# Kernel tuning notes

Hardware: AMD Instinct MI355X
Metric: run time of the kernel (lower is better)

The kernel has to match this reference:

```python
import jax, jax.numpy as jnp
import numpy as np

N = 100000      # num_nodes
E = 1600000     # num_edges (avg degree 16)
D_IN = 128
D_H = 128
D_OUT = 128


def _init_linear(key, out_dim, in_dim):
    # Kaiming-uniform-like init, bound = 1/sqrt(fan_in)
    bound = 1.0 / np.sqrt(in_dim)
    return jax.random.uniform(key, (out_dim, in_dim), jnp.float32, -bound, bound)


def setup_inputs() -> dict:
    key = jax.random.key(0)
    ks = jax.random.split(key, 12)
    x = jax.random.normal(ks[0], (N, D_IN), jnp.float32)
    edge_index = jax.random.randint(ks[1], (2, E), 0, N, jnp.int32)
    dims = [(D_H, D_IN), (D_H, D_H), (D_OUT, D_H)]
    inp = {"x": x, "edge_index": edge_index}
    for i, (do, di) in enumerate(dims):
        inp[f"Wl{i}"] = _init_linear(ks[2 + 3 * i], do, di)      # lin_l: applied to aggregated neighbors
        inp[f"bl{i}"] = jnp.zeros((do,), jnp.float32)
        inp[f"Wr{i}"] = _init_linear(ks[3 + 3 * i], do, di)      # lin_r: applied to root (self) features
    return inp


def _sage_conv(x, src, dst, Wl, bl, Wr):
    # mean aggregation of source-node features at destination nodes
    msg = x[src]                                                   # [E, d]
    agg = jax.ops.segment_sum(msg, dst, num_segments=N)            # [N, d]
    deg = jax.ops.segment_sum(jnp.ones((src.shape[0],), x.dtype), dst, num_segments=N)
    mean = agg / jnp.maximum(deg, 1.0)[:, None]
    return mean @ Wl.T + bl + x @ Wr.T


def reference(x, edge_index, Wl0, bl0, Wr0, Wl1, bl1, Wr1, Wl2, bl2, Wr2):
    src, dst = edge_index[0], edge_index[1]
    # dropout is identity in eval mode
    h = jax.nn.relu(_sage_conv(x, src, dst, Wl0, bl0, Wr0))
    h = jax.nn.relu(_sage_conv(h, src, dst, Wl1, bl1, Wr1))
    return _sage_conv(h, src, dst, Wl2, bl2, Wr2)
```

## Files before the change

### kernel.cpp

```cpp
#include <hip/hip_runtime.h>
#include <hip/hip_bf16.h>

typedef __attribute__((ext_vector_type(8))) short bf16x8;
typedef __attribute__((ext_vector_type(4))) float f32x4;
typedef __attribute__((ext_vector_type(2))) float f32x2;

#define D 128
#define BCAP 8192
#define EPB 3125
#define SBMAX 512


__global__ __launch_bounds__(256) void k_mega(
    const float* __restrict__ x,
    const float* __restrict__ w0, const float* __restrict__ w1,
    const float* __restrict__ w2, const float* __restrict__ w3,
    const float* __restrict__ w4, const float* __restrict__ w5,
    __hip_bfloat16* __restrict__ xb, __hip_bfloat16* __restrict__ wb,
    __hip_bfloat16* __restrict__ h0,
    int* __restrict__ gbuf, int* __restrict__ runinfo,
    const int* __restrict__ src, const int* __restrict__ dst,
    int xquad, int e, int n, int p1b)
{
    if (blockIdx.x < p1b) {
        __shared__ int lh[512], lpre[512], pscan[256];
        __shared__ int lout[3328];
        int t = threadIdx.x;
        lh[t] = 0; lh[t + 256] = 0;
        __syncthreads();
        int lo = blockIdx.x * EPB;
        int hi = lo + EPB; if (hi > e) hi = e;
        for (int i = lo + t; i < hi; i += 256) {
            int d = dst[i]; d = ((unsigned)d < (unsigned)n) ? d : 0;
            atomicAdd(&lh[d >> 8], 1);
        }
        __syncthreads();
        int c0 = lh[2 * t], c1 = lh[2 * t + 1];
        int pair = c0 + c1;
        pscan[t] = pair;
        __syncthreads();
        for (int off = 1; off < 256; off <<= 1) {
            int v = (t >= off) ? pscan[t - off] : 0;
            __syncthreads();
            pscan[t] += v;
            __syncthreads();
        }
        int excl = pscan[t] - pair;
        lpre[2 * t] = excl;
        lpre[2 * t + 1] = excl + c0;
        runinfo[(2 * t) * SBMAX + blockIdx.x]     = (excl << 16) | c0;
        runinfo[(2 * t + 1) * SBMAX + blockIdx.x] = ((excl + c0) << 16) | c1;
        lh[2 * t] = 0; lh[2 * t + 1] = 0;
        __syncthreads();
        for (int i = lo + t; i < hi; i += 256) {
            int d = dst[i]; d = ((unsigned)d < (unsigned)n) ? d : 0;
            int s = src[i]; s = ((unsigned)s < (unsigned)n) ? s : 0;
            int b = d >> 8;
            int p = lpre[b] + atomicAdd(&lh[b], 1);
            lout[p] = s | ((d & 255) << 17);
        }
        __syncthreads();
        int cnt = hi - lo;
        for (int i = t; i < cnt; i += 256) gbuf[lo + i] = lout[i];
    } else {
        int t = (blockIdx.x - p1b) * 256 + threadIdx.x;
        if (t < xquad) {
            float4 f = ((const float4*)x)[t];
            union { int2 i2; __hip_bfloat162 h2[2]; } u;
            u.h2[0] = __float22bfloat162_rn(make_float2(f.x, f.y));
            u.h2[1] = __float22bfloat162_rn(make_float2(f.z, f.w));
            ((int2*)xb)[t] = u.i2;
        }
        if (t < 6 * 4096) {
            int wsel = t >> 12, wi = t & 4095;
            const float* wp = w0;
            if (wsel == 1) wp = w1;
            else if (wsel == 2) wp = w2;
            else if (wsel == 3) wp = w3;
            else if (wsel == 4) wp = w4;
            else if (wsel == 5) wp = w5;
            float4 f = ((const float4*)wp)[wi];
            union { int2 i2; __hip_bfloat162 h2[2]; } u;
            u.h2[0] = __float22bfloat162_rn(make_float2(f.x, f.y));
            u.h2[1] = __float22bfloat162_rn(make_float2(f.z, f.w));
            ((int2*)wb)[t] = u.i2;
        }
        if (t < 16) {
            ((int4*)(xb + (size_t)n * D))[t] = make_int4(0, 0, 0, 0);
            ((int4*)(h0 + (size_t)n * D))[t] = make_int4(0, 0, 0, 0);
        }
    }
}


__global__ __launch_bounds__(256) void k_p2(
    const int* __restrict__ gbuf, const int* __restrict__ runinfo,
    int2* __restrict__ ndesc,
    int* __restrict__ csr, int n, int p1b)
{
    __shared__ int ebuf[BCAP];
    __shared__ int out[BCAP];
    __shared__ int pscan[256];
    __shared__ int hist[256], loc[256], cur[256];
    int b = blockIdx.x, t = threadIdx.x;

    int sb0 = 2 * t, sb1 = 2 * t + 1;
    int r0 = (sb0 < p1b) ? runinfo[b * SBMAX + sb0] : 0;
    int r1 = (sb1 < p1b) ? runinfo[b * SBMAX + sb1] : 0;
    int l0 = r0 & 0xffff, l1 = r1 & 0xffff;
    int pair = l0 + l1;
    pscan[t] = pair;
    __syncthreads();
    for (int off = 1; off < 256; off <<= 1) {
        int v = (t >= off) ? pscan[t - off] : 0;
        __syncthreads();
        pscan[t] += v;
        __syncthreads();
    }
    int excl = pscan[t] - pair;
    int cnt = pscan[255];
    if (cnt > BCAP) cnt = BCAP;

    if (excl < BCAP) {
        int s0 = sb0 * EPB + (r0 >> 16);
        int lim0 = (excl + l0 <= BCAP) ? l0 : (BCAP - excl);
        for (int k = 0; k < lim0; ++k) ebuf[excl + k] = gbuf[s0 + k];
        int o1 = excl + l0;
        if (o1 < BCAP) {
            int s1 = sb1 * EPB + (r1 >> 16);
            int lim1 = (o1 + l1 <= BCAP) ? l1 : (BCAP - o1);
            for (int k = 0; k < lim1; ++k) ebuf[o1 + k] = gbuf[s1 + k];
        }
    }
    __syncthreads();

    int nodes = n - b * 256; if (nodes > 256) nodes = 256;
    hist[t] = 0;
    __syncthreads();
    for (int i = t; i < cnt; i += 256)
        atomicAdd(&hist[(ebuf[i] >> 17) & 255], 1);
    __syncthreads();
    int v = hist[t];
    int pv = (v + 15) & ~15;
    loc[t] = pv;
    __syncthreads();
    for (int off = 1; off < 256; off <<= 1) {
        int x = (t >= off) ? loc[t - off] : 0;
        __syncthreads();
        loc[t] += x;
        __syncthreads();
    }
    int myloc = loc[t] - pv;
    int ptot = loc[255];
    if (ptot > BCAP) ptot = BCAP;
    cur[t] = myloc;
    if (t < nodes) ndesc[b * 256 + t] = make_int2(b * BCAP + myloc, v);
    __syncthreads();
    for (int i = t; i < ptot; i += 256) out[i] = n;
    __syncthreads();
    for (int i = t; i < cnt; i += 256) {
        int ed = ebuf[i];
        int p = atomicAdd(&cur[(ed >> 17) & 255], 1);
        if (p < BCAP) out[p] = ed & 0x1FFFF;
    }
    __syncthreads();
    for (int i = t; i < ptot; i += 256) csr[b * BCAP + i] = out[i];
}


__device__ __forceinline__ void acc_u32(f32x2& a, unsigned p) {
    f32x2 c;
    c.x = __uint_as_float(p << 16);
    c.y = __uint_as_float(p & 0xffff0000u);
    a += c;
}

__device__ __forceinline__ void acc_i4(f32x2* acc, int4 d) {
    acc_u32(acc[0], (unsigned)d.x);
    acc_u32(acc[1], (unsigned)d.y);
    acc_u32(acc[2], (unsigned)d.z);
    acc_u32(acc[3], (unsigned)d.w);
}

__global__ __launch_bounds__(256) void k_agg(
    const __hip_bfloat16* __restrict__ h,
    const int* __restrict__ csr,
    const int2* __restrict__ ndesc,
    __hip_bfloat16* __restrict__ mean,
    int n)
{
    int node = blockIdx.x * 4 + (threadIdx.x >> 6);
    int lane = threadIdx.x & 63;
    if (node >= n) return;
    int grp = lane >> 4;
    int sub = lane & 15;
    int2 nd = ndesc[node];
    int start = nd.x, cnt = nd.y;
    int cntp = (cnt + 15) & ~15;

    f32x2 acc[4];
    #pragma unroll
    for (int k = 0; k < 4; ++k) acc[k] = (f32x2){0.f, 0.f};

    const char* hb = (const char*)h;
    unsigned suboff = (unsigned)sub * 16u;
    const int* cp = csr + start + grp;

    for (int i = 0; i < cntp; i += 16) {
        int s[4];
        #pragma unroll
        for (int u = 0; u < 4; ++u) s[u] = cp[i + u * 4];
        int4 d[4];
        #pragma unroll
        for (int u = 0; u < 4; ++u)
            d[u] = *(const int4*)(hb + (((unsigned)s[u] << 8) | suboff));
        #pragma unroll
        for (int u = 0; u < 4; ++u) acc_i4(acc, d[u]);
    }

    #pragma unroll
    for (int k = 0; k < 4; ++k) {
        acc[k].x += __shfl_xor(acc[k].x, 16);
        acc[k].y += __shfl_xor(acc[k].y, 16);
        acc[k].x += __shfl_xor(acc[k].x, 32);
        acc[k].y += __shfl_xor(acc[k].y, 32);
    }

    if (grp == 0) {
        float inv = 1.0f / fmaxf((float)cnt, 1.0f);
        union { int4 i4; __hip_bfloat162 h2[4]; } u;
        #pragma unroll
        for (int k = 0; k < 4; ++k)
            u.h2[k] = __float22bfloat162_rn(make_float2(acc[k].x * inv, acc[k].y * inv));
        *(int4*)((char*)mean + (size_t)node * 256 + suboff) = u.i4;
    }
}


__global__ __launch_bounds__(512) void k_gemm(
    const __hip_bfloat16* __restrict__ A0,
    const __hip_bfloat16* __restrict__ A1,
    const __hip_bfloat16* __restrict__ Wb,
    const float* __restrict__ bias,
    float* __restrict__ outF,
    __hip_bfloat16* __restrict__ outB,
    int n, int do_relu)
{
    __shared__ __hip_bfloat16 lW[2 * 128 * 128];

    for (int g = threadIdx.x; g < 4096; g += 512) {
        int half = g >> 11;
        int rem  = g & 2047;
        int row  = rem >> 4;
        int c    = rem & 15;
        bf16x8 v = *(const bf16x8*)(Wb + half * 16384 + row * 128 + c * 8);
        *(bf16x8*)(lW + half * 16384 + row * 128 + ((c ^ (row & 7)) * 8)) = v;
    }
    __syncthreads();

    int w = threadIdx.x >> 6;
    int lane = threadIdx.x & 63;
    int m = lane & 15;
    int q = lane >> 4;
    int base = blockIdx.x * 256 + w * 32;

    f32x4 acc[2][8];
    #pragma unroll
    for (int r = 0; r < 2; ++r)
        #pragma unroll
        for (int i = 0; i < 8; ++i) acc[r][i] = (f32x4){0.f, 0.f, 0.f, 0.f};

    const __hip_bfloat16* Aps[2] = {A0, A1};

    #pragma unroll
    for (int half = 0; half < 2; ++half) {
        const __hip_bfloat16* A = Aps[half];
        #pragma unroll
        for (int kk = 0; kk < 4; ++kk) {
            bf16x8 af[2];
            #pragma unroll
            for (int r = 0; r < 2; ++r) {
                int arow = base + r * 16 + m;
                if (arow > n - 1) arow = n - 1;
                af[r] = *(const bf16x8*)(A + (size_t)arow * D + kk * 32 + q * 8);
            }
            #pragma unroll
            for (int nt = 0; nt < 8; ++nt) {
                int row = nt * 16 + m;
                int c = (kk * 4 + q) ^ (m & 7);
                bf16x8 bf = *(const bf16x8*)(lW + half * 16384 + row * 128 + c * 8);
                #pragma unroll
                for (int r = 0; r < 2; ++r)
                    acc[r][nt] = __builtin_amdgcn_mfma_f32_16x16x32_bf16(af[r], bf, acc[r][nt], 0, 0, 0);
            }
        }
    }

    #pragma unroll
    for (int r = 0; r < 2; ++r) {
        #pragma unroll
        for (int nt = 0; nt < 8; ++nt) {
            int col = nt * 16 + m;
            float b = bias[col];
            #pragma unroll
            for (int rr = 0; rr < 4; ++rr) {
                int row = base + r * 16 + q * 4 + rr;
                if (row < n) {
                    float v = acc[r][nt][rr] + b;
                    if (do_relu) v = fmaxf(v, 0.f);
                    if (outF) outF[(size_t)row * D + col] = v;
                    else      outB[(size_t)row * D + col] = __float2bfloat16(v);
                }
            }
        }
    }
}


extern "C" void kernel_launch(void* const* d_in, const int* in_sizes, int n_in,
                              void* d_out, int out_size, void* d_ws, size_t ws_size,
                              hipStream_t stream) {
    const float* x   = (const float*)d_in[0];
    const int*   ei  = (const int*)d_in[1];
    const float* Wl0 = (const float*)d_in[2];
    const float* bl0 = (const float*)d_in[3];
    const float* Wr0 = (const float*)d_in[4];
    const float* Wl1 = (const float*)d_in[5];
    const float* bl1 = (const float*)d_in[6];
    const float* Wr1 = (const float*)d_in[7];
    const float* Wl2 = (const float*)d_in[8];
    const float* bl2 = (const float*)d_in[9];
    const float* Wr2 = (const float*)d_in[10];

    const int n = in_sizes[0] / D;
    const int e = in_sizes[1] / 2;
    const int* src = ei;
    const int* dst = ei + e;
    const int nb = (n + 255) >> 8;

    uintptr_t p = ((uintptr_t)d_ws + 255) & ~(uintptr_t)255;
    auto carve = [&](size_t bytes) {
        uintptr_t r = p;
        p = (p + bytes + 255) & ~(uintptr_t)255;
        return (void*)r;
    };
    int2* ndesc  = (int2*)carve((size_t)n * 8);
    __hip_bfloat16* mean = (__hip_bfloat16*)carve((size_t)n * D * 2);
    __hip_bfloat16* F1   = (__hip_bfloat16*)carve((size_t)(n + 1) * D * 2);
    __hip_bfloat16* Wb   = (__hip_bfloat16*)carve((size_t)6 * D * D * 2);
    (void)ws_size; (void)n_in; (void)out_size;

    char* ob = (char*)d_out;
    __hip_bfloat16* h0 = (__hip_bfloat16*)ob;
    size_t hbytes = (size_t)(n + 1) * D * 2;
    int* gbuf    = (int*)(ob + hbytes);
    int* runinfo = (int*)(ob + hbytes + (size_t)e * 4);
    int* csrS    = (int*)(ob + hbytes + (size_t)e * 4 + (size_t)SBMAX * 512 * 4);

    const int xquad = n * D / 4;
    const int p1b = (e + EPB - 1) / EPB;

    const int megag = p1b + (xquad + 255) / 256;
    k_mega<<<megag, 256, 0, stream>>>(
        x, Wl0, Wr0, Wl1, Wr1, Wl2, Wr2, F1, Wb, h0, gbuf, runinfo, src, dst,
        xquad, e, n, p1b);

    k_p2<<<nb, 256, 0, stream>>>(gbuf, runinfo, ndesc, csrS, n, p1b);

    const int ag = (n + 3) / 4;
    const int gg = (n + 255) / 256;

    __hip_bfloat16* Wb0 = Wb + 0 * 2 * D * D;
    __hip_bfloat16* Wb1 = Wb + 1 * 2 * D * D;
    __hip_bfloat16* Wb2 = Wb + 2 * 2 * D * D;

    k_agg<<<ag, 256, 0, stream>>>(F1, csrS, ndesc, mean, n);
    k_gemm<<<gg, 512, 0, stream>>>(mean, F1, Wb0, bl0, nullptr, h0, n, 1);
    k_agg<<<ag, 256, 0, stream>>>(h0, csrS, ndesc, mean, n);
    k_gemm<<<gg, 512, 0, stream>>>(mean, h0, Wb1, bl1, nullptr, F1, n, 1);
    k_agg<<<ag, 256, 0, stream>>>(F1, csrS, ndesc, mean, n);
    k_gemm<<<gg, 512, 0, stream>>>(mean, F1, Wb2, bl2, (float*)d_out, nullptr, n, 0);
}
```

Baseline: 370.7 us.

## Pre-swizzle weights into MFMA fragment order and drop LDS staging in GEMM

The weight conversion in the mega kernel now writes bf16 weights directly in the per-lane MFMA B-fragment order. The GEMM kernel then loads B fragments straight from global memory (served mostly from L2/L1), so it no longer fills a 64KB LDS tile and syncs. The GEMM block is halved to 256 threads covering 128 rows, with an occupancy hint. This removes the per-block LDS fill and barrier overhead and the LDS occupancy limit, but adds repeated global or cache loads of the weights per wave.

```diff
diff --git a/kernel.cpp b/kernel.cpp
--- a/kernel.cpp
+++ b/kernel.cpp
@@ -71,19 +71,28 @@
             u.h2[1] = __float22bfloat162_rn(make_float2(f.z, f.w));
             ((int2*)xb)[t] = u.i2;
         }
-        if (t < 6 * 4096) {
-            int wsel = t >> 12, wi = t & 4095;
+        if (t < 6 * 2048) {
+            int mat   = t >> 11;
+            int piece = t & 2047;
+            int kk = piece >> 9;
+            int nt = (piece >> 6) & 7;
+            int l  = piece & 63;
+            int row = nt * 16 + (l & 15);
+            int col = kk * 32 + (l >> 4) * 8;
             const float* wp = w0;
-            if (wsel == 1) wp = w1;
-            else if (wsel == 2) wp = w2;
-            else if (wsel == 3) wp = w3;
-            else if (wsel == 4) wp = w4;
-            else if (wsel == 5) wp = w5;
-            float4 f = ((const float4*)wp)[wi];
-            union { int2 i2; __hip_bfloat162 h2[2]; } u;
-            u.h2[0] = __float22bfloat162_rn(make_float2(f.x, f.y));
-            u.h2[1] = __float22bfloat162_rn(make_float2(f.z, f.w));
-            ((int2*)wb)[t] = u.i2;
+            if (mat == 1) wp = w1;
+            else if (mat == 2) wp = w2;
+            else if (mat == 3) wp = w3;
+            else if (mat == 4) wp = w4;
+            else if (mat == 5) wp = w5;
+            const float4* s4 = (const float4*)(wp + row * 128 + col);
+            float4 f0 = s4[0], f1 = s4[1];
+            union { bf16x8 v; __hip_bfloat162 h2[4]; } u;
+            u.h2[0] = __float22bfloat162_rn(make_float2(f0.x, f0.y));
+            u.h2[1] = __float22bfloat162_rn(make_float2(f0.z, f0.w));
+            u.h2[2] = __float22bfloat162_rn(make_float2(f1.x, f1.y));
+            u.h2[3] = __float22bfloat162_rn(make_float2(f1.z, f1.w));
+            *(bf16x8*)(wb + mat * 16384 + piece * 8) = u.v;
         }
         if (t < 16) {
             ((int4*)(xb + (size_t)n * D))[t] = make_int4(0, 0, 0, 0);
@@ -237,32 +246,20 @@
 }
 
 
-__global__ __launch_bounds__(512) void k_gemm(
+__global__ __launch_bounds__(256, 4) void k_gemm(
     const __hip_bfloat16* __restrict__ A0,
     const __hip_bfloat16* __restrict__ A1,
-    const __hip_bfloat16* __restrict__ Wb,
+    const __hip_bfloat16* __restrict__ WbF,
     const float* __restrict__ bias,
     float* __restrict__ outF,
     __hip_bfloat16* __restrict__ outB,
     int n, int do_relu)
 {
-    __shared__ __hip_bfloat16 lW[2 * 128 * 128];
-
-    for (int g = threadIdx.x; g < 4096; g += 512) {
-        int half = g >> 11;
-        int rem  = g & 2047;
-        int row  = rem >> 4;
-        int c    = rem & 15;
-        bf16x8 v = *(const bf16x8*)(Wb + half * 16384 + row * 128 + c * 8);
-        *(bf16x8*)(lW + half * 16384 + row * 128 + ((c ^ (row & 7)) * 8)) = v;
-    }
-    __syncthreads();
-
     int w = threadIdx.x >> 6;
     int lane = threadIdx.x & 63;
     int m = lane & 15;
     int q = lane >> 4;
-    int base = blockIdx.x * 256 + w * 32;
+    int base = blockIdx.x * 128 + w * 32;
 
     f32x4 acc[2][8];
     #pragma unroll
@@ -275,6 +272,7 @@
     #pragma unroll
     for (int half = 0; half < 2; ++half) {
         const __hip_bfloat16* A = Aps[half];
+        const __hip_bfloat16* Wf = WbF + half * 16384 + lane * 8;
         #pragma unroll
         for (int kk = 0; kk < 4; ++kk) {
             bf16x8 af[2];
@@ -286,9 +284,7 @@
             }
             #pragma unroll
             for (int nt = 0; nt < 8; ++nt) {
-                int row = nt * 16 + m;
-                int c = (kk * 4 + q) ^ (m & 7);
-                bf16x8 bf = *(const bf16x8*)(lW + half * 16384 + row * 128 + c * 8);
+                bf16x8 bf = *(const bf16x8*)(Wf + (kk * 512 + nt * 64) * 8);
                 #pragma unroll
                 for (int r = 0; r < 2; ++r)
                     acc[r][nt] = __builtin_amdgcn_mfma_f32_16x16x32_bf16(af[r], bf, acc[r][nt], 0, 0, 0);
@@ -368,16 +364,16 @@
     k_p2<<<nb, 256, 0, stream>>>(gbuf, runinfo, ndesc, csrS, n, p1b);
 
     const int ag = (n + 3) / 4;
-    const int gg = (n + 255) / 256;
+    const int gg = (n + 127) / 128;
 
     __hip_bfloat16* Wb0 = Wb + 0 * 2 * D * D;
     __hip_bfloat16* Wb1 = Wb + 1 * 2 * D * D;
     __hip_bfloat16* Wb2 = Wb + 2 * 2 * D * D;
 
     k_agg<<<ag, 256, 0, stream>>>(F1, csrS, ndesc, mean, n);
-    k_gemm<<<gg, 512, 0, stream>>>(mean, F1, Wb0, bl0, nullptr, h0, n, 1);
+    k_gemm<<<gg, 256, 0, stream>>>(mean, F1, Wb0, bl0, nullptr, h0, n, 1);
     k_agg<<<ag, 256, 0, stream>>>(h0, csrS, ndesc, mean, n);
-    k_gemm<<<gg, 512, 0, stream>>>(mean, h0, Wb1, bl1, nullptr, F1, n, 1);
+    k_gemm<<<gg, 256, 0, stream>>>(mean, h0, Wb1, bl1, nullptr, F1, n, 1);
     k_agg<<<ag, 256, 0, stream>>>(F1, csrS, ndesc, mean, n);
-    k_gemm<<<gg, 512, 0, stream>>>(mean, F1, Wb2, bl2, (float*)d_out, nullptr, n, 0);
-}
+    k_gemm<<<gg, 256, 0, stream>>>(mean, F1, Wb2, bl2, (float*)d_out, nullptr, n, 0);
+}
```

After: 389.5 us. 5.1% more time.

## Shrink GEMM tiles to 64 rows with staged half-weight LDS and move buffers to workspace

Applied to the files above, without the earlier changes.

The fused GEMM now uses 256-thread blocks covering 64 rows, with each wave computing one 16-row tile. It stages only half of the weight matrix (32 KB) in LDS at a time and reloads it between the neighbor half and the self half. The aim is to raise occupancy and the number of blocks in flight (about 1563 instead of 391), at the cost of loading weights more often per output row and an extra barrier. Scratch buffers (h0, gbuf, runinfo, csrS) move from the output buffer into the workspace, which also removes the aliasing of h0 with the final output.

```diff
diff --git a/kernel.cpp b/kernel.cpp
--- a/kernel.cpp
+++ b/kernel.cpp
@@ -237,7 +237,7 @@
 }
 
 
-__global__ __launch_bounds__(512) void k_gemm(
+__global__ __launch_bounds__(256) void k_gemm(
     const __hip_bfloat16* __restrict__ A0,
     const __hip_bfloat16* __restrict__ A1,
     const __hip_bfloat16* __restrict__ Wb,
@@ -246,71 +246,59 @@
     __hip_bfloat16* __restrict__ outB,
     int n, int do_relu)
 {
-    __shared__ __hip_bfloat16 lW[2 * 128 * 128];
-
-    for (int g = threadIdx.x; g < 4096; g += 512) {
-        int half = g >> 11;
-        int rem  = g & 2047;
-        int row  = rem >> 4;
-        int c    = rem & 15;
-        bf16x8 v = *(const bf16x8*)(Wb + half * 16384 + row * 128 + c * 8);
-        *(bf16x8*)(lW + half * 16384 + row * 128 + ((c ^ (row & 7)) * 8)) = v;
-    }
-    __syncthreads();
+    __shared__ __hip_bfloat16 lW[128 * 128];
 
     int w = threadIdx.x >> 6;
     int lane = threadIdx.x & 63;
     int m = lane & 15;
     int q = lane >> 4;
-    int base = blockIdx.x * 256 + w * 32;
-
-    f32x4 acc[2][8];
-    #pragma unroll
-    for (int r = 0; r < 2; ++r)
-        #pragma unroll
-        for (int i = 0; i < 8; ++i) acc[r][i] = (f32x4){0.f, 0.f, 0.f, 0.f};
+    int base = blockIdx.x * 64 + w * 16;
+    int arow = base + m;
+    if (arow > n - 1) arow = n - 1;
+
+    f32x4 acc[8];
+    #pragma unroll
+    for (int i = 0; i < 8; ++i) acc[i] = (f32x4){0.f, 0.f, 0.f, 0.f};
 
     const __hip_bfloat16* Aps[2] = {A0, A1};
 
     #pragma unroll
     for (int half = 0; half < 2; ++half) {
+        if (half) __syncthreads();
+        for (int g = threadIdx.x; g < 2048; g += 256) {
+            int row = g >> 4;
+            int c   = g & 15;
+            bf16x8 v = *(const bf16x8*)(Wb + half * 16384 + row * 128 + c * 8);
+            *(bf16x8*)(lW + row * 128 + ((c ^ (row & 7)) * 8)) = v;
+        }
+        __syncthreads();
+
         const __hip_bfloat16* A = Aps[half];
         #pragma unroll
         for (int kk = 0; kk < 4; ++kk) {
-            bf16x8 af[2];
-            #pragma unroll
-            for (int r = 0; r < 2; ++r) {
-                int arow = base + r * 16 + m;
-                if (arow > n - 1) arow = n - 1;
-                af[r] = *(const bf16x8*)(A + (size_t)arow * D + kk * 32 + q * 8);
-            }
+            bf16x8 af = *(const bf16x8*)(A + (size_t)arow * D + kk * 32 + q * 8);
             #pragma unroll
             for (int nt = 0; nt < 8; ++nt) {
                 int row = nt * 16 + m;
                 int c = (kk * 4 + q) ^ (m & 7);
-                bf16x8 bf = *(const bf16x8*)(lW + half * 16384 + row * 128 + c * 8);
-                #pragma unroll
-                for (int r = 0; r < 2; ++r)
-                    acc[r][nt] = __builtin_amdgcn_mfma_f32_16x16x32_bf16(af[r], bf, acc[r][nt], 0, 0, 0);
+                bf16x8 bf = *(const bf16x8*)(lW + row * 128 + c * 8);
+                acc[nt] = __builtin_amdgcn_mfma_f32_16x16x32_bf16(af, bf, acc[nt], 0, 0, 0);
             }
         }
     }
 
     #pragma unroll
-    for (int r = 0; r < 2; ++r) {
-        #pragma unroll
-        for (int nt = 0; nt < 8; ++nt) {
-            int col = nt * 16 + m;
-            float b = bias[col];
-            #pragma unroll
-            for (int rr = 0; rr < 4; ++rr) {
-                int row = base + r * 16 + q * 4 + rr;
-                if (row < n) {
-                    float v = acc[r][nt][rr] + b;
-                    if (do_relu) v = fmaxf(v, 0.f);
-                    if (outF) outF[(size_t)row * D + col] = v;
-                    else      outB[(size_t)row * D + col] = __float2bfloat16(v);
-                }
+    for (int nt = 0; nt < 8; ++nt) {
+        int col = nt * 16 + m;
+        float b = bias[col];
+        #pragma unroll
+        for (int rr = 0; rr < 4; ++rr) {
+            int row = base + q * 4 + rr;
+            if (row < n) {
+                float v = acc[nt][rr] + b;
+                if (do_relu) v = fmaxf(v, 0.f);
+                if (outF) outF[(size_t)row * D + col] = v;
+                else      outB[(size_t)row * D + col] = __float2bfloat16(v);
             }
         }
     }
@@ -347,15 +335,12 @@
     int2* ndesc  = (int2*)carve((size_t)n * 8);
     __hip_bfloat16* mean = (__hip_bfloat16*)carve((size_t)n * D * 2);
     __hip_bfloat16* F1   = (__hip_bfloat16*)carve((size_t)(n + 1) * D * 2);
+    __hip_bfloat16* h0   = (__hip_bfloat16*)carve((size_t)(n + 1) * D * 2);
     __hip_bfloat16* Wb   = (__hip_bfloat16*)carve((size_t)6 * D * D * 2);
+    int* gbuf    = (int*)carve((size_t)e * 4);
+    int* runinfo = (int*)carve((size_t)SBMAX * 512 * 4);
+    int* csrS    = (int*)carve((size_t)nb * BCAP * 4);
     (void)ws_size; (void)n_in; (void)out_size;
-
-    char* ob = (char*)d_out;
-    __hip_bfloat16* h0 = (__hip_bfloat16*)ob;
-    size_t hbytes = (size_t)(n + 1) * D * 2;
-    int* gbuf    = (int*)(ob + hbytes);
-    int* runinfo = (int*)(ob + hbytes + (size_t)e * 4);
-    int* csrS    = (int*)(ob + hbytes + (size_t)e * 4 + (size_t)SBMAX * 512 * 4);
 
     const int xquad = n * D / 4;
     const int p1b = (e + EPB - 1) / EPB;
@@ -368,16 +353,16 @@
     k_p2<<<nb, 256, 0, stream>>>(gbuf, runinfo, ndesc, csrS, n, p1b);
 
     const int ag = (n + 3) / 4;
-    const int gg = (n + 255) / 256;
+    const int gg = (n + 63) / 64;
 
     __hip_bfloat16* Wb0 = Wb + 0 * 2 * D * D;
     __hip_bfloat16* Wb1 = Wb + 1 * 2 * D * D;
     __hip_bfloat16* Wb2 = Wb + 2 * 2 * D * D;
 
     k_agg<<<ag, 256, 0, stream>>>(F1, csrS, ndesc, mean, n);
-    k_gemm<<<gg, 512, 0, stream>>>(mean, F1, Wb0, bl0, nullptr, h0, n, 1);
+    k_gemm<<<gg, 256, 0, stream>>>(mean, F1, Wb0, bl0, nullptr, h0, n, 1);
     k_agg<<<ag, 256, 0, stream>>>(h0, csrS, ndesc, mean, n);
-    k_gemm<<<gg, 512, 0, stream>>>(mean, h0, Wb1, bl1, nullptr, F1, n, 1);
+    k_gemm<<<gg, 256, 0, stream>>>(mean, h0, Wb1, bl1, nullptr, F1, n, 1);
     k_agg<<<ag, 256, 0, stream>>>(F1, csrS, ndesc, mean, n);
-    k_gemm<<<gg, 512, 0, stream>>>(mean, F1, Wb2, bl2, (float*)d_out, nullptr, n, 0);
-}
+    k_gemm<<<gg, 256, 0, stream>>>(mean, F1, Wb2, bl2, (float*)d_out, nullptr, n, 0);
+}
```

After: 393.8 us. +6.2%, slower.
